# Performance work log

Hardware: AMD Instinct MI355X
Metric: run time of the kernel (lower is better)

The kernel has to match this reference:

```python
import jax, jax.numpy as jnp
import numpy as np

PATCH_ORIG = (5, 15, 15)
DWS = [(1, 4, 4), (1, 2, 2), (1, 1, 1)]
STRIDE = [(1, 6, 6), (1, 6, 6), (1, 3, 3)]
EMBED = 32
EPS = 1e-6


def _extract_full_patches(x, shape, stride):
    # x: (N,C,D,H,W) -> (N*P, C, *shape) patches (torch unfold + permute + view)
    N, C = x.shape[:2]
    sp = x.shape[2:]
    nb = tuple((sp[i] - shape[i]) // stride[i] + 1 for i in range(3))
    d = (jnp.arange(nb[0]) * stride[0])[:, None] + jnp.arange(shape[0])[None, :]
    h = (jnp.arange(nb[1]) * stride[1])[:, None] + jnp.arange(shape[1])[None, :]
    w = (jnp.arange(nb[2]) * stride[2])[:, None] + jnp.arange(shape[2])[None, :]
    pat = x[:, :, d[:, None, None, :, None, None],
                  h[None, :, None, None, :, None],
                  w[None, None, :, None, None, :]]
    # (N, C, nb0, nb1, nb2, p0, p1, p2) -> (N*P, C, p0, p1, p2)
    pat = pat.transpose(0, 2, 3, 4, 1, 5, 6, 7).reshape(-1, C, *shape)
    return pat, nb


def _extract_centers(x, stride, offset, nb):
    # 1x1x1 patches at fixed crop offset, limited to nb -> (N*P, C)
    sl = x[:, :, offset[0]::stride[0], offset[1]::stride[1], offset[2]::stride[2]]
    sl = sl[:, :, :nb[0], :nb[1], :nb[2]]
    N, C = sl.shape[:2]
    return sl.transpose(0, 2, 3, 4, 1).reshape(-1, C)


def _maxpool(x, fct):
    # MaxPool3d(kernel=stride=fct) on exactly-divisible dims via reshape trick
    B, C = x.shape[:2]
    p0, p1, p2 = x.shape[2] // fct[0], x.shape[3] // fct[1], x.shape[4] // fct[2]
    x = x.reshape(B, C, p0, fct[0], p1, fct[1], p2, fct[2])
    return x.max(axis=(3, 5, 7))


def _dice(pred, trg):
    # inferno SorensenDiceLoss, channelwise: flatten to (C, -1)
    p = pred.transpose(1, 0, 2, 3, 4).reshape(pred.shape[1], -1)
    t = trg.transpose(1, 0, 2, 3, 4).reshape(trg.shape[1], -1)
    num = (p * t).sum(-1)
    den = jnp.clip((p * p + t * t).sum(-1), EPS, None)
    return (-2.0 * num / den).sum()


def _level_loss(pred, target, W, b, lvl):
    gt = target[:, :1].astype(jnp.float32)           # GT label volume (N,1,D,H,W)
    affs = target[:, 1:].astype(jnp.float32)
    bnd = 1.0 - affs
    bmask = bnd[:, 4:].max(1, keepdims=True) if lvl == 0 else bnd[:, :4].max(1, keepdims=True)
    dws, stride = DWS[lvl], STRIDE[lvl]
    pshape = tuple(p * f for p, f in zip(PATCH_ORIG, dws))
    off = tuple(s // 2 for s in pshape)              # crop offset (rnd crop fixed to 0)

    gt_patches, nb = _extract_full_patches(gt, pshape, stride)   # (P,1,*pshape)
    centers = _extract_centers(gt, stride, off, nb)[:, 0]        # (P,)
    on_bnd = _extract_centers(bmask, stride, off, nb)[:, 0]      # (P,)

    me = (gt_patches != centers[:, None, None, None, None]).astype(jnp.float32)
    ign = (gt_patches == 0).astype(jnp.float32)
    valid = ((centers != 0) & (on_bnd != 1.0)).astype(jnp.float32)

    trg = _maxpool(me, dws)                                      # (P,1,*PATCH_ORIG)
    ign_m = _maxpool(ign, dws) > 0

    emb = _extract_centers(pred, stride, off, nb)                # (P, EMBED)
    pp = jax.nn.sigmoid(emb @ W + b).reshape(-1, 1, *PATCH_ORIG) # patch decoder

    pp = jnp.where(ign_m, 0.0, pp)
    trg = jnp.where(ign_m, 0.0, trg)
    v = valid[:, None, None, None, None]                         # mask == select valid patches for sum-based Dice
    return _dice(pp * v, trg * v)


def setup_inputs() -> dict:
    key = jax.random.key(0)
    ks = jax.random.split(key, 16)
    shapes = [(2, 8, 160, 160), (2, 8, 80, 80), (2, 8, 40, 40)]
    inp = {}
    for lvl, (n, d, hh, ww) in enumerate(shapes):
        inp[f'pred{lvl}'] = jax.random.normal(ks[lvl], (n, EMBED, d, hh, ww), jnp.float32)
        gt = jax.random.randint(ks[3 + lvl], (n, 1, d, hh, ww), 0, 50, jnp.int32)
        affs = jax.random.randint(ks[6 + lvl], (n, 8, d, hh, ww), 0, 2, jnp.int32)
        inp[f'tgt{lvl}'] = jnp.concatenate([gt, affs], axis=1)
        inp[f'W{lvl}'] = 0.1 * jax.random.normal(ks[9 + lvl], (EMBED, int(np.prod(PATCH_ORIG))), jnp.float32)
        inp[f'b{lvl}'] = jnp.zeros((int(np.prod(PATCH_ORIG)),), jnp.float32)
    return inp


def reference(pred0, pred1, pred2, W0, b0, W1, b1, W2, b2, tgt0, tgt1, tgt2):
    loss = _level_loss(pred0, tgt0, W0, b0, 0)
    loss = loss + _level_loss(pred1, tgt1, W1, b1, 1)
    loss = loss + _level_loss(pred2, tgt2, W2, b2, 2)
    return loss
```

## Files before the change

### kernel.cpp

```cpp
#include <hip/hip_runtime.h>
#include <hip/hip_bf16.h>


constexpr int NBATCH = 2;
constexpr int EMB = 32;
constexpr int TGTC = 9;
constexpr int PZ = 5, PY = 15, PX = 15;
constexpr int P = PZ * PY * PX;

constexpr int NBLK0 = NBATCH * 4 * 17 * 17;
constexpr int NBLK1 = NBATCH * 4 * 9 * 9;
constexpr int NBLK2 = NBATCH * 4 * 9 * 9;
constexpr int NBLK_TOT = NBLK0 + NBLK1 + NBLK2;

template <int D, int H, int W,
          int NB0, int NBH, int NBW,
          int SH, int SW,
          int DH, int DWIN,
          int OFFZ, int OFFY, int OFFX,
          int AFFB>
__device__ __forceinline__
void level_body(const int lbid,
                const float* __restrict__ pred,
                const int* __restrict__ tgt,
                const float* __restrict__ Wm,
                const float* __restrict__ bv,
                float* __restrict__ partials)
{
    const int tid = threadIdx.x;

    int k  = lbid % NBW;
    int t1 = lbid / NBW;
    int j  = t1 % NBH;
    int t2 = t1 / NBH;
    int i  = t2 % NB0;
    int b  = t2 / NB0;

    const int HW = H * W;
    const int CH = D * HW;
    const int zc = OFFZ + i;
    const int yc = OFFY + j * SH;
    const int xc = OFFX + k * SW;
    const int cidx = zc * HW + yc * W + xc;

    __shared__ float s_emb[EMB];
    __shared__ int   s_c;
    __shared__ int   s_valid;

    if (tid == 0) {
        const int c = tgt[b * TGTC * CH + cidx];
        bool allaff = true;
        #pragma unroll
        for (int ch = 0; ch < 4; ++ch)
            allaff &= (tgt[(b * TGTC + AFFB + ch) * CH + cidx] != 0);
        s_c = c;
        s_valid = (c != 0) && allaff;
    }
    __syncthreads();

    if (!s_valid) {
        if (tid == 0) {
            partials[2 * lbid]     = 0.0f;
            partials[2 * lbid + 1] = 0.0f;
        }
        return;
    }

    if (tid < EMB)
        s_emb[tid] = pred[(b * EMB + tid) * CH + cidx];
    __syncthreads();

    const int* __restrict__ gtb = tgt + b * TGTC * CH;
    const int c = s_c;

    float num = 0.0f, den = 0.0f;
    for (int o = tid; o < P; o += 256) {
        const int pz = o / (PY * PX);
        const int r  = o - pz * (PY * PX);
        const int py = r / PX;
        const int px = r - py * PX;

        float dot = bv[o];
        #pragma unroll
        for (int e = 0; e < EMB; ++e)
            dot = fmaf(s_emb[e], Wm[e * P + o], dot);
        float pp = __builtin_amdgcn_rcpf(1.0f + __expf(-dot));

        const int zb = i + pz;
        const int yb = j * SH + py * DH;
        const int xb = k * SW + px * DWIN;
        bool anyz = false, anyd = false;
        #pragma unroll
        for (int wy = 0; wy < DH; ++wy) {
            #pragma unroll
            for (int wx = 0; wx < DWIN; ++wx) {
                const int g = gtb[zb * HW + (yb + wy) * W + (xb + wx)];
                anyz |= (g == 0);
                anyd |= (g != c);
            }
        }
        float trg = (anyz || !anyd) ? 0.0f : 1.0f;
        if (anyz) pp = 0.0f;

        num = fmaf(pp, trg, num);
        den += pp * pp + trg * trg;
    }

    #pragma unroll
    for (int off = 32; off > 0; off >>= 1) {
        num += __shfl_down(num, off);
        den += __shfl_down(den, off);
    }
    __shared__ float sn[4], sd[4];
    if ((tid & 63) == 0) { sn[tid >> 6] = num; sd[tid >> 6] = den; }
    __syncthreads();
    if (tid == 0) {
        partials[2 * lbid]     = sn[0] + sn[1] + sn[2] + sn[3];
        partials[2 * lbid + 1] = sd[0] + sd[1] + sd[2] + sd[3];
    }
}

__global__ __launch_bounds__(256)
void stage_kernel(const float* __restrict__ pred0, const int* __restrict__ tgt0,
                  const float* __restrict__ W0, const float* __restrict__ b0,
                  const float* __restrict__ pred1, const int* __restrict__ tgt1,
                  const float* __restrict__ W1, const float* __restrict__ b1,
                  const float* __restrict__ pred2, const int* __restrict__ tgt2,
                  const float* __restrict__ W2, const float* __restrict__ b2,
                  float* __restrict__ partials)
{
    const int gb = blockIdx.x;
    if (gb < NBLK0) {
        level_body<8, 160, 160, 4, 17, 17, 6, 6, 4, 4, 2, 30, 30, 5>(
            gb, pred0, tgt0, W0, b0, partials);
    } else if (gb < NBLK0 + NBLK1) {
        level_body<8, 80, 80, 4, 9, 9, 6, 6, 2, 2, 2, 15, 15, 1>(
            gb - NBLK0, pred1, tgt1, W1, b1, partials + 2 * NBLK0);
    } else {
        level_body<8, 40, 40, 4, 9, 9, 3, 3, 1, 1, 2, 7, 7, 1>(
            gb - NBLK0 - NBLK1, pred2, tgt2, W2, b2,
            partials + 2 * (NBLK0 + NBLK1));
    }
}

__global__ __launch_bounds__(256)
void finalize_kernel(const float* __restrict__ partials, float* __restrict__ out)
{
    const int tid = threadIdx.x;

    float n0 = 0.f, d0 = 0.f, n1 = 0.f, d1 = 0.f, n2 = 0.f, d2 = 0.f;
    const float2* p2 = (const float2*)partials;
    #pragma unroll 4
    for (int p = tid; p < NBLK_TOT; p += 256) {
        const float2 v = p2[p];
        if (p < NBLK0)              { n0 += v.x; d0 += v.y; }
        else if (p < NBLK0 + NBLK1) { n1 += v.x; d1 += v.y; }
        else                        { n2 += v.x; d2 += v.y; }
    }

    #pragma unroll
    for (int off = 32; off > 0; off >>= 1) {
        n0 += __shfl_down(n0, off);  d0 += __shfl_down(d0, off);
        n1 += __shfl_down(n1, off);  d1 += __shfl_down(d1, off);
        n2 += __shfl_down(n2, off);  d2 += __shfl_down(d2, off);
    }
    __shared__ float s[4][6];
    if ((tid & 63) == 0) {
        const int w = tid >> 6;
        s[w][0] = n0; s[w][1] = d0; s[w][2] = n1;
        s[w][3] = d1; s[w][4] = n2; s[w][5] = d2;
    }
    __syncthreads();
    if (tid == 0) {
        float acc[6];
        #pragma unroll
        for (int q = 0; q < 6; ++q)
            acc[q] = s[0][q] + s[1][q] + s[2][q] + s[3][q];
        float loss = 0.0f;
        loss += -2.0f * acc[0] / fmaxf(acc[1], 1e-6f);
        loss += -2.0f * acc[2] / fmaxf(acc[3], 1e-6f);
        loss += -2.0f * acc[4] / fmaxf(acc[5], 1e-6f);
        out[0] = loss;
    }
}

extern "C" void kernel_launch(void* const* d_in, const int* in_sizes, int n_in,
                              void* d_out, int out_size, void* d_ws, size_t ws_size,
                              hipStream_t stream)
{
    const float* pred0 = (const float*)d_in[0];
    const int*   tgt0  = (const int*)  d_in[1];
    const float* W0    = (const float*)d_in[2];
    const float* b0    = (const float*)d_in[3];
    const float* pred1 = (const float*)d_in[4];
    const int*   tgt1  = (const int*)  d_in[5];
    const float* W1    = (const float*)d_in[6];
    const float* b1    = (const float*)d_in[7];
    const float* pred2 = (const float*)d_in[8];
    const int*   tgt2  = (const int*)  d_in[9];
    const float* W2    = (const float*)d_in[10];
    const float* b2    = (const float*)d_in[11];

    float* out      = (float*)d_out;
    float* partials = (float*)d_ws;

    stage_kernel<<<NBLK_TOT, 256, 0, stream>>>(
        pred0, tgt0, W0, b0, pred1, tgt1, W1, b1, pred2, tgt2, W2, b2,
        partials);
    finalize_kernel<<<1, 256, 0, stream>>>(partials, out);
}
```

Before: 19.91 us.

## Map one wavefront per patch instead of one block per patch

Each patch is now processed by a single 64-lane wavefront, with four patches packed into a 256-thread block. Shared-memory staging and block barriers are replaced by register broadcasts via shuffles and an xor-shuffle reduction. Each lane now handles about 18 outputs instead of about 5, which lengthens per-wave serial work but removes barrier and launch overhead. Invalid patches now exit per wave rather than leaving a whole block mostly idle. The finalize kernel reads partials as float4.

After: 29.95 us. +50.4%, slower.

```diff
diff --git a/kernel.cpp b/kernel.cpp
--- a/kernel.cpp
+++ b/kernel.cpp
@@ -20,14 +20,14 @@
           int OFFZ, int OFFY, int OFFX,
           int AFFB>
 __device__ __forceinline__
-void level_body(const int lbid,
-                const float* __restrict__ pred,
-                const int* __restrict__ tgt,
-                const float* __restrict__ Wm,
-                const float* __restrict__ bv,
-                float* __restrict__ partials)
-{
-    const int tid = threadIdx.x;
+void wave_pb(const int lbid,
+             const float* __restrict__ pred,
+             const int* __restrict__ tgt,
+             const float* __restrict__ Wm,
+             const float* __restrict__ bv,
+             float* __restrict__ partials)
+{
+    const int lane = threadIdx.x & 63;
 
     int k  = lbid % NBW;
     int t1 = lbid / NBW;
@@ -43,80 +43,74 @@
     const int xc = OFFX + k * SW;
     const int cidx = zc * HW + yc * W + xc;
 
-    __shared__ float s_emb[EMB];
-    __shared__ int   s_c;
-    __shared__ int   s_valid;
-
-    if (tid == 0) {
-        const int c = tgt[b * TGTC * CH + cidx];
-        bool allaff = true;
-        #pragma unroll
-        for (int ch = 0; ch < 4; ++ch)
-            allaff &= (tgt[(b * TGTC + AFFB + ch) * CH + cidx] != 0);
-        s_c = c;
-        s_valid = (c != 0) && allaff;
-    }
-    __syncthreads();
-
-    if (!s_valid) {
-        if (tid == 0) {
+    const int c = tgt[b * TGTC * CH + cidx];
+    bool allaff = true;
+    #pragma unroll
+    for (int ch = 0; ch < 4; ++ch)
+        allaff &= (tgt[(b * TGTC + AFFB + ch) * CH + cidx] != 0);
+    const bool valid = (c != 0) && allaff;
+
+    if (!valid) {
+        if (lane == 0) {
             partials[2 * lbid]     = 0.0f;
             partials[2 * lbid + 1] = 0.0f;
         }
         return;
     }
 
-    if (tid < EMB)
-        s_emb[tid] = pred[(b * EMB + tid) * CH + cidx];
-    __syncthreads();
+    const float me = pred[(b * EMB + (lane & 31)) * CH + cidx];
+    float ev[EMB];
+    #pragma unroll
+    for (int e = 0; e < EMB; ++e)
+        ev[e] = __shfl(me, e);
 
     const int* __restrict__ gtb = tgt + b * TGTC * CH;
-    const int c = s_c;
 
     float num = 0.0f, den = 0.0f;
-    for (int o = tid; o < P; o += 256) {
-        const int pz = o / (PY * PX);
-        const int r  = o - pz * (PY * PX);
-        const int py = r / PX;
-        const int px = r - py * PX;
-
-        float dot = bv[o];
-        #pragma unroll
-        for (int e = 0; e < EMB; ++e)
-            dot = fmaf(s_emb[e], Wm[e * P + o], dot);
-        float pp = __builtin_amdgcn_rcpf(1.0f + __expf(-dot));
-
-        const int zb = i + pz;
-        const int yb = j * SH + py * DH;
-        const int xb = k * SW + px * DWIN;
-        bool anyz = false, anyd = false;
-        #pragma unroll
-        for (int wy = 0; wy < DH; ++wy) {
+    constexpr int NIT = (P + 63) / 64;
+    for (int it = 0; it < NIT; ++it) {
+        const int o = lane + 64 * it;
+        if (o < P) {
+            const int pz = o / (PY * PX);
+            const int r  = o - pz * (PY * PX);
+            const int py = r / PX;
+            const int px = r - py * PX;
+
+            float dot = bv[o];
             #pragma unroll
-            for (int wx = 0; wx < DWIN; ++wx) {
-                const int g = gtb[zb * HW + (yb + wy) * W + (xb + wx)];
-                anyz |= (g == 0);
-                anyd |= (g != c);
+            for (int e = 0; e < EMB; ++e)
+                dot = fmaf(ev[e], Wm[e * P + o], dot);
+            float pp = __builtin_amdgcn_rcpf(1.0f + __expf(-dot));
+
+            const int zb = i + pz;
+            const int yb = j * SH + py * DH;
+            const int xb = k * SW + px * DWIN;
+            bool anyz = false, anyd = false;
+            #pragma unroll
+            for (int wy = 0; wy < DH; ++wy) {
+                #pragma unroll
+                for (int wx = 0; wx < DWIN; ++wx) {
+                    const int g = gtb[zb * HW + (yb + wy) * W + (xb + wx)];
+                    anyz |= (g == 0);
+                    anyd |= (g != c);
+                }
             }
+            float trg = (anyz || !anyd) ? 0.0f : 1.0f;
+            if (anyz) pp = 0.0f;
+
+            num = fmaf(pp, trg, num);
+            den += pp * pp + trg * trg;
         }
-        float trg = (anyz || !anyd) ? 0.0f : 1.0f;
-        if (anyz) pp = 0.0f;
-
-        num = fmaf(pp, trg, num);
-        den += pp * pp + trg * trg;
     }
 
     #pragma unroll
     for (int off = 32; off > 0; off >>= 1) {
-        num += __shfl_down(num, off);
-        den += __shfl_down(den, off);
-    }
-    __shared__ float sn[4], sd[4];
-    if ((tid & 63) == 0) { sn[tid >> 6] = num; sd[tid >> 6] = den; }
-    __syncthreads();
-    if (tid == 0) {
-        partials[2 * lbid]     = sn[0] + sn[1] + sn[2] + sn[3];
-        partials[2 * lbid + 1] = sd[0] + sd[1] + sd[2] + sd[3];
+        num += __shfl_xor(num, off);
+        den += __shfl_xor(den, off);
+    }
+    if (lane == 0) {
+        partials[2 * lbid]     = num;
+        partials[2 * lbid + 1] = den;
     }
 }
 
@@ -129,16 +123,16 @@
                   const float* __restrict__ W2, const float* __restrict__ b2,
                   float* __restrict__ partials)
 {
-    const int gb = blockIdx.x;
-    if (gb < NBLK0) {
-        level_body<8, 160, 160, 4, 17, 17, 6, 6, 4, 4, 2, 30, 30, 5>(
-            gb, pred0, tgt0, W0, b0, partials);
-    } else if (gb < NBLK0 + NBLK1) {
-        level_body<8, 80, 80, 4, 9, 9, 6, 6, 2, 2, 2, 15, 15, 1>(
-            gb - NBLK0, pred1, tgt1, W1, b1, partials + 2 * NBLK0);
+    const int pb = blockIdx.x * 4 + (threadIdx.x >> 6);
+    if (pb < NBLK0) {
+        wave_pb<8, 160, 160, 4, 17, 17, 6, 6, 4, 4, 2, 30, 30, 5>(
+            pb, pred0, tgt0, W0, b0, partials);
+    } else if (pb < NBLK0 + NBLK1) {
+        wave_pb<8, 80, 80, 4, 9, 9, 6, 6, 2, 2, 2, 15, 15, 1>(
+            pb - NBLK0, pred1, tgt1, W1, b1, partials + 2 * NBLK0);
     } else {
-        level_body<8, 40, 40, 4, 9, 9, 3, 3, 1, 1, 2, 7, 7, 1>(
-            gb - NBLK0 - NBLK1, pred2, tgt2, W2, b2,
+        wave_pb<8, 40, 40, 4, 9, 9, 3, 3, 1, 1, 2, 7, 7, 1>(
+            pb - NBLK0 - NBLK1, pred2, tgt2, W2, b2,
             partials + 2 * (NBLK0 + NBLK1));
     }
 }
@@ -148,14 +142,17 @@
 {
     const int tid = threadIdx.x;
 
+    constexpr int NF4 = NBLK_TOT / 2;
+    constexpr int B01 = NBLK0 / 2;
+    constexpr int B12 = (NBLK0 + NBLK1) / 2;
+
     float n0 = 0.f, d0 = 0.f, n1 = 0.f, d1 = 0.f, n2 = 0.f, d2 = 0.f;
-    const float2* p2 = (const float2*)partials;
-    #pragma unroll 4
-    for (int p = tid; p < NBLK_TOT; p += 256) {
-        const float2 v = p2[p];
-        if (p < NBLK0)              { n0 += v.x; d0 += v.y; }
-        else if (p < NBLK0 + NBLK1) { n1 += v.x; d1 += v.y; }
-        else                        { n2 += v.x; d2 += v.y; }
+    const float4* p4 = (const float4*)partials;
+    for (int p = tid; p < NF4; p += 256) {
+        const float4 v = p4[p];
+        if (p < B01)      { n0 += v.x + v.z; d0 += v.y + v.w; }
+        else if (p < B12) { n1 += v.x + v.z; d1 += v.y + v.w; }
+        else              { n2 += v.x + v.z; d2 += v.y + v.w; }
     }
 
     #pragma unroll
@@ -204,7 +201,7 @@
     float* out      = (float*)d_out;
     float* partials = (float*)d_ws;
 
-    stage_kernel<<<NBLK_TOT, 256, 0, stream>>>(
+    stage_kernel<<<NBLK_TOT / 4, 256, 0, stream>>>(
         pred0, tgt0, W0, b0, pred1, tgt1, W1, b1, pred2, tgt2, W2, b2,
         partials);
     finalize_kernel<<<1, 256, 0, stream>>>(partials, out);
```

## Process eight patches per block and vectorize finalize reduction loads

Applied to the files above, without the earlier changes.

Each workgroup now handles eight patch centers instead of one. It loads all validity and center values in parallel up front, then loops over the valid patches with the same dot-product and boundary logic. The grid shrinks eightfold, which cuts block launch and scheduling overhead for the many invalid patches. The cost is serialized work inside each block and fewer blocks spread across the CUs. The finalize kernel also reads partials as float4, two patches per load.

New measurement: 25.18 us. 26.4% more time.

```diff
diff --git a/kernel.cpp b/kernel.cpp
--- a/kernel.cpp
+++ b/kernel.cpp
@@ -12,6 +12,12 @@
 constexpr int NBLK1 = NBATCH * 4 * 9 * 9;
 constexpr int NBLK2 = NBATCH * 4 * 9 * 9;
 constexpr int NBLK_TOT = NBLK0 + NBLK1 + NBLK2;
+
+constexpr int PBB = 8;
+constexpr int NB0_B = NBLK0 / PBB;
+constexpr int NB1_B = NBLK1 / PBB;
+constexpr int NB2_B = NBLK2 / PBB;
+constexpr int NBLK_B = NB0_B + NB1_B + NB2_B;
 
 template <int D, int H, int W,
           int NB0, int NBH, int NBW,
@@ -20,103 +26,115 @@
           int OFFZ, int OFFY, int OFFX,
           int AFFB>
 __device__ __forceinline__
-void level_body(const int lbid,
-                const float* __restrict__ pred,
-                const int* __restrict__ tgt,
-                const float* __restrict__ Wm,
-                const float* __restrict__ bv,
-                float* __restrict__ partials)
+void block8(const int blk,
+            const float* __restrict__ pred,
+            const int* __restrict__ tgt,
+            const float* __restrict__ Wm,
+            const float* __restrict__ bv,
+            float* __restrict__ partials)
 {
     const int tid = threadIdx.x;
-
-    int k  = lbid % NBW;
-    int t1 = lbid / NBW;
-    int j  = t1 % NBH;
-    int t2 = t1 / NBH;
-    int i  = t2 % NB0;
-    int b  = t2 / NB0;
-
-    const int HW = H * W;
-    const int CH = D * HW;
-    const int zc = OFFZ + i;
-    const int yc = OFFY + j * SH;
-    const int xc = OFFX + k * SW;
-    const int cidx = zc * HW + yc * W + xc;
-
+    constexpr int HW = H * W;
+    constexpr int CH = D * HW;
+
+    __shared__ int   s_val[PBB][5];
+    __shared__ int   s_meta[PBB][4];
+    __shared__ int   s_valid[PBB];
+    __shared__ int   s_c[PBB];
     __shared__ float s_emb[EMB];
-    __shared__ int   s_c;
-    __shared__ int   s_valid;
-
-    if (tid == 0) {
-        const int c = tgt[b * TGTC * CH + cidx];
-        bool allaff = true;
+    __shared__ float sn[4], sd[4];
+
+    if (tid < PBB * 5) {
+        const int s = tid / 5, q = tid % 5;
+        const int pb = blk * PBB + s;
+        int k  = pb % NBW;
+        int t1 = pb / NBW;
+        int j  = t1 % NBH;
+        int t2 = t1 / NBH;
+        int i  = t2 % NB0;
+        int b  = t2 / NB0;
+        const int cidx = (OFFZ + i) * HW + (OFFY + j * SH) * W + (OFFX + k * SW);
+        const int ch = (q == 0) ? 0 : (AFFB + q - 1);
+        s_val[s][q] = tgt[(b * TGTC + ch) * CH + cidx];
+        if (q == 0) {
+            s_meta[s][0] = b; s_meta[s][1] = i;
+            s_meta[s][2] = j; s_meta[s][3] = k;
+        }
+    }
+    __syncthreads();
+    if (tid < PBB) {
+        const int c = s_val[tid][0];
+        const bool v = (c != 0) & (s_val[tid][1] != 0) & (s_val[tid][2] != 0)
+                                & (s_val[tid][3] != 0) & (s_val[tid][4] != 0);
+        s_valid[tid] = v;
+        s_c[tid] = c;
+        if (!v) {
+            const int pb = blk * PBB + tid;
+            partials[2 * pb]     = 0.0f;
+            partials[2 * pb + 1] = 0.0f;
+        }
+    }
+    __syncthreads();
+
+    for (int s = 0; s < PBB; ++s) {
+        if (!s_valid[s]) continue;
+
+        const int b = s_meta[s][0], i = s_meta[s][1];
+        const int j = s_meta[s][2], k = s_meta[s][3];
+        const int cidx = (OFFZ + i) * HW + (OFFY + j * SH) * W + (OFFX + k * SW);
+        if (tid < EMB)
+            s_emb[tid] = pred[(b * EMB + tid) * CH + cidx];
+        __syncthreads();
+
+        const int c = s_c[s];
+        const int* __restrict__ gtb = tgt + b * TGTC * CH;
+
+        float num = 0.0f, den = 0.0f;
+        for (int o = tid; o < P; o += 256) {
+            const int pz = o / (PY * PX);
+            const int r  = o - pz * (PY * PX);
+            const int py = r / PX;
+            const int px = r - py * PX;
+
+            float dot = bv[o];
+            #pragma unroll
+            for (int e = 0; e < EMB; ++e)
+                dot = fmaf(s_emb[e], Wm[e * P + o], dot);
+            float pp = __builtin_amdgcn_rcpf(1.0f + __expf(-dot));
+
+            const int zb = i + pz;
+            const int yb = j * SH + py * DH;
+            const int xb = k * SW + px * DWIN;
+            bool anyz = false, anyd = false;
+            #pragma unroll
+            for (int wy = 0; wy < DH; ++wy) {
+                #pragma unroll
+                for (int wx = 0; wx < DWIN; ++wx) {
+                    const int g = gtb[zb * HW + (yb + wy) * W + (xb + wx)];
+                    anyz |= (g == 0);
+                    anyd |= (g != c);
+                }
+            }
+            float trg = (anyz || !anyd) ? 0.0f : 1.0f;
+            if (anyz) pp = 0.0f;
+
+            num = fmaf(pp, trg, num);
+            den += pp * pp + trg * trg;
+        }
+
         #pragma unroll
-        for (int ch = 0; ch < 4; ++ch)
-            allaff &= (tgt[(b * TGTC + AFFB + ch) * CH + cidx] != 0);
-        s_c = c;
-        s_valid = (c != 0) && allaff;
-    }
-    __syncthreads();
-
-    if (!s_valid) {
+        for (int off = 32; off > 0; off >>= 1) {
+            num += __shfl_xor(num, off);
+            den += __shfl_xor(den, off);
+        }
+        if ((tid & 63) == 0) { sn[tid >> 6] = num; sd[tid >> 6] = den; }
+        __syncthreads();
         if (tid == 0) {
-            partials[2 * lbid]     = 0.0f;
-            partials[2 * lbid + 1] = 0.0f;
-        }
-        return;
-    }
-
-    if (tid < EMB)
-        s_emb[tid] = pred[(b * EMB + tid) * CH + cidx];
-    __syncthreads();
-
-    const int* __restrict__ gtb = tgt + b * TGTC * CH;
-    const int c = s_c;
-
-    float num = 0.0f, den = 0.0f;
-    for (int o = tid; o < P; o += 256) {
-        const int pz = o / (PY * PX);
-        const int r  = o - pz * (PY * PX);
-        const int py = r / PX;
-        const int px = r - py * PX;
-
-        float dot = bv[o];
-        #pragma unroll
-        for (int e = 0; e < EMB; ++e)
-            dot = fmaf(s_emb[e], Wm[e * P + o], dot);
-        float pp = __builtin_amdgcn_rcpf(1.0f + __expf(-dot));
-
-        const int zb = i + pz;
-        const int yb = j * SH + py * DH;
-        const int xb = k * SW + px * DWIN;
-        bool anyz = false, anyd = false;
-        #pragma unroll
-        for (int wy = 0; wy < DH; ++wy) {
-            #pragma unroll
-            for (int wx = 0; wx < DWIN; ++wx) {
-                const int g = gtb[zb * HW + (yb + wy) * W + (xb + wx)];
-                anyz |= (g == 0);
-                anyd |= (g != c);
-            }
-        }
-        float trg = (anyz || !anyd) ? 0.0f : 1.0f;
-        if (anyz) pp = 0.0f;
-
-        num = fmaf(pp, trg, num);
-        den += pp * pp + trg * trg;
-    }
-
-    #pragma unroll
-    for (int off = 32; off > 0; off >>= 1) {
-        num += __shfl_down(num, off);
-        den += __shfl_down(den, off);
-    }
-    __shared__ float sn[4], sd[4];
-    if ((tid & 63) == 0) { sn[tid >> 6] = num; sd[tid >> 6] = den; }
-    __syncthreads();
-    if (tid == 0) {
-        partials[2 * lbid]     = sn[0] + sn[1] + sn[2] + sn[3];
-        partials[2 * lbid + 1] = sd[0] + sd[1] + sd[2] + sd[3];
+            const int pb = blk * PBB + s;
+            partials[2 * pb]     = sn[0] + sn[1] + sn[2] + sn[3];
+            partials[2 * pb + 1] = sd[0] + sd[1] + sd[2] + sd[3];
+        }
+        __syncthreads();
     }
 }
 
@@ -130,15 +148,15 @@
                   float* __restrict__ partials)
 {
     const int gb = blockIdx.x;
-    if (gb < NBLK0) {
-        level_body<8, 160, 160, 4, 17, 17, 6, 6, 4, 4, 2, 30, 30, 5>(
+    if (gb < NB0_B) {
+        block8<8, 160, 160, 4, 17, 17, 6, 6, 4, 4, 2, 30, 30, 5>(
             gb, pred0, tgt0, W0, b0, partials);
-    } else if (gb < NBLK0 + NBLK1) {
-        level_body<8, 80, 80, 4, 9, 9, 6, 6, 2, 2, 2, 15, 15, 1>(
-            gb - NBLK0, pred1, tgt1, W1, b1, partials + 2 * NBLK0);
+    } else if (gb < NB0_B + NB1_B) {
+        block8<8, 80, 80, 4, 9, 9, 6, 6, 2, 2, 2, 15, 15, 1>(
+            gb - NB0_B, pred1, tgt1, W1, b1, partials + 2 * NBLK0);
     } else {
-        level_body<8, 40, 40, 4, 9, 9, 3, 3, 1, 1, 2, 7, 7, 1>(
-            gb - NBLK0 - NBLK1, pred2, tgt2, W2, b2,
+        block8<8, 40, 40, 4, 9, 9, 3, 3, 1, 1, 2, 7, 7, 1>(
+            gb - NB0_B - NB1_B, pred2, tgt2, W2, b2,
             partials + 2 * (NBLK0 + NBLK1));
     }
 }
@@ -148,14 +166,17 @@
 {
     const int tid = threadIdx.x;
 
+    constexpr int NF4 = NBLK_TOT / 2;
+    constexpr int B01 = NBLK0 / 2;
+    constexpr int B12 = (NBLK0 + NBLK1) / 2;
+
     float n0 = 0.f, d0 = 0.f, n1 = 0.f, d1 = 0.f, n2 = 0.f, d2 = 0.f;
-    const float2* p2 = (const float2*)partials;
-    #pragma unroll 4
-    for (int p = tid; p < NBLK_TOT; p += 256) {
-        const float2 v = p2[p];
-        if (p < NBLK0)              { n0 += v.x; d0 += v.y; }
-        else if (p < NBLK0 + NBLK1) { n1 += v.x; d1 += v.y; }
-        else                        { n2 += v.x; d2 += v.y; }
+    const float4* p4 = (const float4*)partials;
+    for (int p = tid; p < NF4; p += 256) {
+        const float4 v = p4[p];
+        if (p < B01)      { n0 += v.x + v.z; d0 += v.y + v.w; }
+        else if (p < B12) { n1 += v.x + v.z; d1 += v.y + v.w; }
+        else              { n2 += v.x + v.z; d2 += v.y + v.w; }
     }
 
     #pragma unroll
@@ -204,7 +225,7 @@
     float* out      = (float*)d_out;
     float* partials = (float*)d_ws;
 
-    stage_kernel<<<NBLK_TOT, 256, 0, stream>>>(
+    stage_kernel<<<NBLK_B, 256, 0, stream>>>(
         pred0, tgt0, W0, b0, pred1, tgt1, W1, b1, pred2, tgt2, W2, b2,
         partials);
     finalize_kernel<<<1, 256, 0, stream>>>(partials, out);
```
